# Performance work log

Measured on AMD Instinct MI355X. Metric: run time of the kernel, lower is better.

## Reference

```python
import jax, jax.numpy as jnp
import numpy as np

# levels for the auction iterations: j = 7..-1 gives level = -4^j, j = -2 gives level = 0
_LEVEL_JS = list(range(7, -3, -1))


def approx_match(xyz1, xyz2):
    # xyz1: [B,N,3], xyz2: [B,M,3] -> soft match matrix [B,N,M]
    B, N, _ = xyz1.shape
    M = xyz2.shape[1]
    multiL = 1.0 if N >= M else float(M // N)
    multiR = float(N // M) if N >= M else 1.0
    # pairwise squared distances [B,N,M]
    d2 = jnp.sum((xyz1[:, :, None, :] - xyz2[:, None, :, :]) ** 2, axis=-1)
    levels = jnp.array([0.0 if j == -2 else -(4.0 ** j) for j in _LEVEL_JS],
                       dtype=xyz1.dtype)

    def step(carry, level):
        match, remainL, remainR = carry
        w = jnp.exp(level * d2) * remainR[:, None, :]                      # [B,N,M]
        # row-normalize to each left point's remaining mass
        w = w * (remainL / (jnp.sum(w, axis=2) + 1e-9))[:, :, None]
        # clip columns to right points' remaining capacity
        ss = jnp.sum(w, axis=1) + 1e-9                                     # [B,M]
        w = w * jnp.minimum(remainR / ss, 1.0)[:, None, :]
        match = match + w
        remainL = jnp.maximum(remainL - jnp.sum(w, axis=2), 0.0)
        remainR = jnp.maximum(remainR - jnp.sum(w, axis=1), 0.0)
        return (match, remainL, remainR), None

    init = (jnp.zeros_like(d2),
            jnp.full((B, N), multiL, dtype=d2.dtype),
            jnp.full((B, M), multiR, dtype=d2.dtype))
    (match, _, _), _ = jax.lax.scan(step, init, levels)
    return match


def match_cost(xyz1, xyz2, match):
    # cost[b] = sum_{k,l} match[b,k,l] * ||xyz1[b,k] - xyz2[b,l]||
    d = jnp.sqrt(jnp.sum((xyz1[:, :, None, :] - xyz2[:, None, :, :]) ** 2, axis=-1))
    return jnp.sum(match * d, axis=(1, 2))


def setup_inputs() -> dict:
    key = jax.random.key(0)
    k1, k2 = jax.random.split(key)
    B, N, M = 8, 2048, 2048
    input1 = jax.random.normal(k1, (B, N, 3), dtype=jnp.float32)
    input2 = jax.random.normal(k2, (B, M, 3), dtype=jnp.float32)
    return {"input1": input1, "input2": input2}


def reference(input1, input2):
    match = approx_match(input1, input2)
    return match_cost(input1, input2, match)
```

## Files before the change

### kernel.cpp

```cpp
#include <hip/hip_runtime.h>
#include <hip/hip_fp16.h>


#define BATCH 8
#define NPTS 2048
#define MPTS 2048
#define BLOCK 256
#define ROWS 16
#define LOG2E 1.44269504088896340736f

__device__ __forceinline__ float fast_exp2(float x) {
  return __builtin_amdgcn_exp2f(x);
}
__device__ __forceinline__ float fast_sqrt(float a) {
  return __builtin_amdgcn_sqrtf(a);
}
__device__ __forceinline__ float packh2(float c, float r) {
  __half2 h = __halves2half2(__float2half_rn(c), __float2half_rn(r));
  return __builtin_bit_cast(float, h);
}

__device__ __forceinline__ void load8(const float4* q, int r0, float k,
                                      float* x, float* y, float* z) {
  int b4 = (r0 >> 2) * 3;
  float4 q0 = q[b4], q1 = q[b4 + 1], q2 = q[b4 + 2];
  float4 q3 = q[b4 + 3], q4 = q[b4 + 4], q5 = q[b4 + 5];
  x[0] = k * q0.x; y[0] = k * q0.y; z[0] = k * q0.z;
  x[1] = k * q0.w; y[1] = k * q1.x; z[1] = k * q1.y;
  x[2] = k * q1.z; y[2] = k * q1.w; z[2] = k * q2.x;
  x[3] = k * q2.y; y[3] = k * q2.z; z[3] = k * q2.w;
  x[4] = k * q3.x; y[4] = k * q3.y; z[4] = k * q3.z;
  x[5] = k * q3.w; y[5] = k * q4.x; z[5] = k * q4.y;
  x[6] = k * q4.z; y[6] = k * q4.w; z[6] = k * q5.x;
  x[7] = k * q5.y; y[7] = k * q5.z; z[7] = k * q5.w;
}

__global__ __launch_bounds__(BLOCK, 4) void emd_A0_kernel(
    const float* __restrict__ xyz1, const float* __restrict__ xyz2,
    float* __restrict__ rowscale, float* __restrict__ out,
    float* __restrict__ t9, float* __restrict__ t1acc,
    float* __restrict__ t1zero, float k0) {
  __shared__ float4 sP[MPTS];
  __shared__ float sRed[ROWS * 4];
  __shared__ float sRs[ROWS];

  const int tid = threadIdx.x;
  const int bid = blockIdx.x;
  const int b = bid >> 7;
  const int t0 = (bid & 127) * ROWS;
  const bool desig = (bid & 127) == 0;
  if (bid == 0 && tid < BATCH) { out[tid] = 0.0f; t9[tid] = 0.0f; }

  const float4* q2 = (const float4*)(xyz2 + (size_t)b * MPTS * 3);
  float4* z4 = (float4*)(t1zero + (size_t)b * MPTS);
  for (int g = tid; g < MPTS / 4; g += BLOCK) {
    float4 a = q2[3 * g], bb = q2[3 * g + 1], c = q2[3 * g + 2];
    sP[4 * g + 0] = make_float4(k0 * a.x, k0 * a.y, k0 * a.z, 0.0f);
    sP[4 * g + 1] = make_float4(k0 * a.w, k0 * bb.x, k0 * bb.y, 0.0f);
    sP[4 * g + 2] = make_float4(k0 * bb.z, k0 * bb.w, k0 * c.x, 0.0f);
    sP[4 * g + 3] = make_float4(k0 * c.y, k0 * c.z, k0 * c.w, 0.0f);
    if (desig) z4[g] = make_float4(0.f, 0.f, 0.f, 0.f);
  }
  __syncthreads();

  const int wave = tid >> 6, lane = tid & 63;
  const int phase = lane >> 1, rg = lane & 1;
  const int r0 = t0 + rg * 8;
  float x1[8], y1[8], z1[8], acc[8];
  load8((const float4*)(xyz1 + (size_t)b * NPTS * 3), r0, k0, x1, y1, z1);
#pragma unroll
  for (int j = 0; j < 8; ++j) acc[j] = 0.0f;
  const int mb = wave * 512 + phase;
#pragma unroll 2
  for (int it = 0; it < 16; ++it) {
    float4 v = sP[mb + it * 32];
#pragma unroll
    for (int j = 0; j < 8; ++j) {
      float dx = x1[j] - v.x, dy = y1[j] - v.y, dz = z1[j] - v.z;
      float s = __builtin_fmaf(dx, dx, __builtin_fmaf(dy, dy, dz * dz));
      acc[j] += fast_exp2(-s);
    }
  }
#pragma unroll
  for (int j = 0; j < 8; ++j) {
    acc[j] += __shfl_xor(acc[j], 2, 64);
    acc[j] += __shfl_xor(acc[j], 4, 64);
    acc[j] += __shfl_xor(acc[j], 8, 64);
    acc[j] += __shfl_xor(acc[j], 16, 64);
    acc[j] += __shfl_xor(acc[j], 32, 64);
  }
  if (lane < 2) {
#pragma unroll
    for (int j = 0; j < 8; ++j) sRed[(rg * 8 + j) * 4 + wave] = acc[j];
  }
  __syncthreads();
  if (tid < ROWS) {
    float s = sRed[tid * 4] + sRed[tid * 4 + 1] + sRed[tid * 4 + 2] +
              sRed[tid * 4 + 3];
    float rs = 1.0f / (s + 1e-9f);
    rowscale[(size_t)b * NPTS + t0 + tid] = rs;
    sRs[tid] = rs;
  }
  __syncthreads();

  float rsn[8];
#pragma unroll
  for (int j = 0; j < 8; ++j) rsn[j] = sRs[rg * 8 + j];
  float* accb = t1acc + (size_t)b * MPTS;
#pragma unroll 2
  for (int it = 0; it < 16; ++it) {
    int idx = mb + it * 32;
    float4 v = sP[idx];
    float part = 0.0f;
#pragma unroll
    for (int j = 0; j < 8; ++j) {
      float dx = x1[j] - v.x, dy = y1[j] - v.y, dz = z1[j] - v.z;
      float s = __builtin_fmaf(dx, dx, __builtin_fmaf(dy, dy, dz * dz));
      part = __builtin_fmaf(fast_exp2(-s), rsn[j], part);
    }
    part += __shfl_xor(part, 1, 64);
    if (rg == 0) atomicAdd(accb + idx, part);
  }
}

template <bool FIRST, bool LAST>
__global__ __launch_bounds__(BLOCK, 4) void emd_CA_kernel(
    const float* __restrict__ xyz1, const float* __restrict__ xyz2,
    float* __restrict__ rowscale, float* __restrict__ remainL,
    const float* __restrict__ rrIn, float* __restrict__ rrOut,
    const float* __restrict__ t1In, float* __restrict__ t1Acc,
    float* __restrict__ t1Zero, float* __restrict__ out,
    float* __restrict__ t9, float kS, float invK) {
  __shared__ float4 sP[MPTS];
  __shared__ float sRedS[ROWS * 4];
  __shared__ float sRedC[ROWS * 4];
  __shared__ float sRedR[ROWS * 4];
  __shared__ float sCost[ROWS];
  __shared__ float sRs[ROWS];

  const int tid = threadIdx.x;
  const int bid = blockIdx.x;
  const int b = bid >> 7;
  const int t0 = (bid & 127) * ROWS;
  const bool desig = (bid & 127) == 0;

  const float4* q2 = (const float4*)(xyz2 + (size_t)b * MPTS * 3);
  const float4* rr4 = (const float4*)(rrIn + (size_t)b * MPTS);
  const float4* t14 = (const float4*)(t1In + (size_t)b * MPTS);
  float4* ro4 = (float4*)(rrOut + (size_t)b * MPTS);
  float4* z4 = LAST ? nullptr : (float4*)(t1Zero + (size_t)b * MPTS);
  for (int g = tid; g < MPTS / 4; g += BLOCK) {
    float4 a = q2[3 * g], bb = q2[3 * g + 1], c = q2[3 * g + 2];
    float4 t1v = t14[g];
    float4 rrv = FIRST ? make_float4(1.f, 1.f, 1.f, 1.f) : rr4[g];
    float cc[4], rn[4];
    float rrc[4] = {rrv.x, rrv.y, rrv.z, rrv.w};
    float t1c[4] = {t1v.x, t1v.y, t1v.z, t1v.w};
#pragma unroll
    for (int i = 0; i < 4; ++i) {
      float colsum = rrc[i] * t1c[i];
      float cs = fminf(rrc[i] / (colsum + 1e-9f), 1.0f);
      cc[i] = rrc[i] * cs;
      rn[i] = fmaxf(rrc[i] - colsum * cs, 0.0f);
    }
    sP[4 * g + 0] = make_float4(kS * a.x, kS * a.y, kS * a.z, packh2(cc[0], rn[0]));
    sP[4 * g + 1] = make_float4(kS * a.w, kS * bb.x, kS * bb.y, packh2(cc[1], rn[1]));
    sP[4 * g + 2] = make_float4(kS * bb.z, kS * bb.w, kS * c.x, packh2(cc[2], rn[2]));
    sP[4 * g + 3] = make_float4(kS * c.y, kS * c.z, kS * c.w, packh2(cc[3], rn[3]));
    if (desig) {
      ro4[g] = make_float4(rn[0], rn[1], rn[2], rn[3]);
      if (!LAST) z4[g] = make_float4(0.f, 0.f, 0.f, 0.f);
    }
  }
  __syncthreads();

  const int wave = tid >> 6, lane = tid & 63;
  const int phase = lane >> 2, rg = lane & 3;
  const int r0 = t0 + rg * 4;
  float x1[4], y1[4], z1[4];
  {
    const float4* q1 = (const float4*)(xyz1 + (size_t)b * NPTS * 3);
    int b4 = (r0 >> 2) * 3;
    float4 a = q1[b4], bb = q1[b4 + 1], c = q1[b4 + 2];
    x1[0] = kS * a.x;  y1[0] = kS * a.y;  z1[0] = kS * a.z;
    x1[1] = kS * a.w;  y1[1] = kS * bb.x; z1[1] = kS * bb.y;
    x1[2] = kS * bb.z; y1[2] = kS * bb.w; z1[2] = kS * c.x;
    x1[3] = kS * c.y;  y1[3] = kS * c.z;  z1[3] = kS * c.w;
  }
  float accS[4] = {0.f, 0.f, 0.f, 0.f};
  float accC[4] = {0.f, 0.f, 0.f, 0.f};
  float accR[4] = {0.f, 0.f, 0.f, 0.f};
  const int mb = wave * 512 + phase;
#pragma unroll 4
  for (int it = 0; it < 32; ++it) {
    float4 v = sP[mb + it * 16];
    __half2 h = __builtin_bit_cast(__half2, v.w);
    float cc = __low2float(h);
    float rr = __high2float(h);
#pragma unroll
    for (int j = 0; j < 4; ++j) {
      float dx = x1[j] - v.x, dy = y1[j] - v.y, dz = z1[j] - v.z;
      float s = __builtin_fmaf(dx, dx, __builtin_fmaf(dy, dy, dz * dz));
      float sq = fast_sqrt(s);
      float e1, e2;
      if (LAST) {
        e2 = 1.0f;
        e1 = fast_exp2(-s);
      } else {
        e2 = fast_exp2(-s);
        float e2s = e2 * e2;
        e1 = e2s * e2s;
      }
      float t = e1 * cc;
      accS[j] += t;
      accC[j] = __builtin_fmaf(t, sq, accC[j]);
      if (LAST) accR[j] += rr;
      else      accR[j] = __builtin_fmaf(e2, rr, accR[j]);
    }
  }
#pragma unroll
  for (int j = 0; j < 4; ++j) {
    accS[j] += __shfl_xor(accS[j], 4, 64);
    accS[j] += __shfl_xor(accS[j], 8, 64);
    accS[j] += __shfl_xor(accS[j], 16, 64);
    accS[j] += __shfl_xor(accS[j], 32, 64);
    accC[j] += __shfl_xor(accC[j], 4, 64);
    accC[j] += __shfl_xor(accC[j], 8, 64);
    accC[j] += __shfl_xor(accC[j], 16, 64);
    accC[j] += __shfl_xor(accC[j], 32, 64);
    accR[j] += __shfl_xor(accR[j], 4, 64);
    accR[j] += __shfl_xor(accR[j], 8, 64);
    accR[j] += __shfl_xor(accR[j], 16, 64);
    accR[j] += __shfl_xor(accR[j], 32, 64);
  }
  if (lane < 4) {
#pragma unroll
    for (int j = 0; j < 4; ++j) {
      sRedS[(rg * 4 + j) * 4 + wave] = accS[j];
      sRedC[(rg * 4 + j) * 4 + wave] = accC[j];
      sRedR[(rg * 4 + j) * 4 + wave] = accR[j];
    }
  }
  __syncthreads();
  if (tid < ROWS) {
    float S2 = sRedS[tid * 4] + sRedS[tid * 4 + 1] + sRedS[tid * 4 + 2] +
               sRedS[tid * 4 + 3];
    float C = sRedC[tid * 4] + sRedC[tid * 4 + 1] + sRedC[tid * 4 + 2] +
              sRedC[tid * 4 + 3];
    float R = sRedR[tid * 4] + sRedR[tid * 4 + 1] + sRedR[tid * 4 + 2] +
              sRedR[tid * 4 + 3];
    size_t idx = (size_t)b * NPTS + t0 + tid;
    float rs = rowscale[idx];
    float rl = FIRST ? 1.0f : remainL[idx];
    float rlN = fmaxf(rl - rs * S2, 0.0f);
    remainL[idx] = rlN;
    float rsN = rlN / (R + 1e-9f);
    rowscale[idx] = rsN;
    sCost[tid] = rs * C * invK;
    sRs[tid] = rsN;
  }
  __syncthreads();
  if (tid == 0) {
    float t = 0.0f;
#pragma unroll
    for (int i = 0; i < ROWS; ++i) t += sCost[i];
    atomicAdd(out + b, t);
    if (LAST) {
      float r = 0.0f;
#pragma unroll
      for (int i = 0; i < ROWS; ++i) r += sRs[i];
      atomicAdd(t9 + b, r);
    }
  }
  if (!LAST) {
    float rsn[4];
#pragma unroll
    for (int j = 0; j < 4; ++j) rsn[j] = sRs[rg * 4 + j];
    float* accb = t1Acc + (size_t)b * MPTS;
#pragma unroll 4
    for (int it = 0; it < 32; ++it) {
      int idx = mb + it * 16;
      float4 v = sP[idx];
      float part = 0.0f;
#pragma unroll
      for (int j = 0; j < 4; ++j) {
        float dx = x1[j] - v.x, dy = y1[j] - v.y, dz = z1[j] - v.z;
        float s = __builtin_fmaf(dx, dx, __builtin_fmaf(dy, dy, dz * dz));
        part = __builtin_fmaf(fast_exp2(-s), rsn[j], part);
      }
      part += __shfl_xor(part, 1, 64);
      part += __shfl_xor(part, 2, 64);
      if (rg == 0) atomicAdd(accb + idx, part);
    }
  }
}

__global__ __launch_bounds__(BLOCK, 4) void emd_C9_kernel(
    const float* __restrict__ xyz1, const float* __restrict__ xyz2,
    const float* __restrict__ rowscale, const float* __restrict__ remainR,
    const float* __restrict__ t9, float* __restrict__ out) {
  __shared__ float4 sP[MPTS];
  __shared__ float sRed[ROWS * 4];
  __shared__ float sCost[ROWS];

  const int tid = threadIdx.x;
  const int bid = blockIdx.x;
  const int b = bid >> 7;
  const int t0 = (bid & 127) * ROWS;
  const int wave = tid >> 6, lane = tid & 63;
  const float t1 = t9[b];

  const float4* q2 = (const float4*)(xyz2 + (size_t)b * MPTS * 3);
  const float4* rr4 = (const float4*)(remainR + (size_t)b * MPTS);
  for (int g = tid; g < MPTS / 4; g += BLOCK) {
    float4 a = q2[3 * g], bb = q2[3 * g + 1], c = q2[3 * g + 2];
    float4 rr = rr4[g];
    float w0 = rr.x * fminf(rr.x / (rr.x * t1 + 1e-9f), 1.0f);
    float w1 = rr.y * fminf(rr.y / (rr.y * t1 + 1e-9f), 1.0f);
    float w2 = rr.z * fminf(rr.z / (rr.z * t1 + 1e-9f), 1.0f);
    float w3 = rr.w * fminf(rr.w / (rr.w * t1 + 1e-9f), 1.0f);
    sP[4 * g + 0] = make_float4(a.x, a.y, a.z, w0);
    sP[4 * g + 1] = make_float4(a.w, bb.x, bb.y, w1);
    sP[4 * g + 2] = make_float4(bb.z, bb.w, c.x, w2);
    sP[4 * g + 3] = make_float4(c.y, c.z, c.w, w3);
  }
  __syncthreads();

  const int phase = lane >> 1, rg = lane & 1;
  const int r0 = t0 + rg * 8;
  float x1[8], y1[8], z1[8], acc[8];
  load8((const float4*)(xyz1 + (size_t)b * NPTS * 3), r0, 1.0f, x1, y1, z1);
#pragma unroll
  for (int j = 0; j < 8; ++j) acc[j] = 0.0f;
  const int mb = wave * 512 + phase;
#pragma unroll 2
  for (int it = 0; it < 16; ++it) {
    float4 v = sP[mb + it * 32];
#pragma unroll
    for (int j = 0; j < 8; ++j) {
      float dx = x1[j] - v.x, dy = y1[j] - v.y, dz = z1[j] - v.z;
      float d2 = __builtin_fmaf(dx, dx, __builtin_fmaf(dy, dy, dz * dz));
      acc[j] = __builtin_fmaf(fast_sqrt(d2), v.w, acc[j]);
    }
  }
#pragma unroll
  for (int j = 0; j < 8; ++j) {
    acc[j] += __shfl_xor(acc[j], 2, 64);
    acc[j] += __shfl_xor(acc[j], 4, 64);
    acc[j] += __shfl_xor(acc[j], 8, 64);
    acc[j] += __shfl_xor(acc[j], 16, 64);
    acc[j] += __shfl_xor(acc[j], 32, 64);
  }
  if (lane < 2) {
#pragma unroll
    for (int j = 0; j < 8; ++j) sRed[(rg * 8 + j) * 4 + wave] = acc[j];
  }
  __syncthreads();
  if (tid < ROWS) {
    float C = sRed[tid * 4] + sRed[tid * 4 + 1] + sRed[tid * 4 + 2] +
              sRed[tid * 4 + 3];
    sCost[tid] = rowscale[(size_t)b * NPTS + t0 + tid] * C;
  }
  __syncthreads();
  if (tid == 0) {
    float t = 0.0f;
#pragma unroll
    for (int i = 0; i < ROWS; ++i) t += sCost[i];
    atomicAdd(out + b, t);
  }
}

extern "C" void kernel_launch(void* const* d_in, const int* in_sizes, int n_in,
                              void* d_out, int out_size, void* d_ws, size_t ws_size,
                              hipStream_t stream) {
  const float* xyz1 = (const float*)d_in[0];
  const float* xyz2 = (const float*)d_in[1];
  float* out = (float*)d_out;
  float* ws = (float*)d_ws;

  const int BN = BATCH * NPTS, BM = BATCH * MPTS;
  float* remainL  = ws;
  float* rowscale = ws + BN;
  float* rrA      = ws + 2 * BN;
  float* rrB      = ws + 2 * BN + BM;
  float* t1b      = ws + 2 * BN + 2 * BM;
  float* t9       = ws + 2 * BN + 5 * BM;

  const float levels[9] = {-16384.f, -4096.f, -1024.f, -256.f, -64.f,
                           -16.f,    -4.f,    -1.f,    -0.25f};
  dim3 grid(BATCH * (NPTS / ROWS));

  hipMemsetAsync(t1b, 0, (size_t)BM * sizeof(float), stream);

  emd_A0_kernel<<<grid, BLOCK, 0, stream>>>(
      xyz1, xyz2, rowscale, out, t9, t1b , t1b + BM ,
      sqrtf(-levels[0] * LOG2E));

  for (int l = 0; l < 9; ++l) {
    float kB = sqrtf(-levels[l] * LOG2E);
    float kA = 0.5f * kB;
    float* cur = t1b + (size_t)(l % 3) * BM;
    float* nxt = t1b + (size_t)((l + 1) % 3) * BM;
    float* zer = t1b + (size_t)((l + 2) % 3) * BM;
    float* rin = (l % 2 == 0) ? rrA : rrB;
    float* rou = (l % 2 == 0) ? rrB : rrA;
    if (l == 0) {
      emd_CA_kernel<true, false><<<grid, BLOCK, 0, stream>>>(
          xyz1, xyz2, rowscale, remainL, rin, rou, cur, nxt, zer, out, t9,
          kA, 1.0f / kA);
    } else if (l < 8) {
      emd_CA_kernel<false, false><<<grid, BLOCK, 0, stream>>>(
          xyz1, xyz2, rowscale, remainL, rin, rou, cur, nxt, zer, out, t9,
          kA, 1.0f / kA);
    } else {
      emd_CA_kernel<false, true><<<grid, BLOCK, 0, stream>>>(
          xyz1, xyz2, rowscale, remainL, rin, rou, cur, nxt, zer, out, t9,
          kB, 1.0f / kB);
    }
  }
  emd_C9_kernel<<<grid, BLOCK, 0, stream>>>(xyz1, xyz2, rowscale, rrB, t9, out);
}
```

Baseline: 357.6 us.

## Fuse all auction levels into one persistent kernel with per-batch grid barriers

Replaces the chain of eleven kernel launches (A0, nine CA levels, C9) with a single persistent kernel. Blocks of the same batch synchronise through atomic counter barriers, and row scale and remaining-left mass stay in shared memory across levels instead of going through global memory. Cross-block data is read and written with agent-scope relaxed atomics. This removes launch gaps and some global traffic. In exchange it needs all 1024 blocks to be co-resident, which the launch bounds of four blocks per CU should allow on a 256-CU device. The spin barrier has a guard that could silently break out early, and there are no acquire/release fences.

```diff
diff --git a/kernel.cpp b/kernel.cpp
--- a/kernel.cpp
+++ b/kernel.cpp
@@ -7,6 +7,8 @@
 #define MPTS 2048
 #define BLOCK 256
 #define ROWS 16
+#define BLOCKS_PER_BATCH 128
+#define NSYNC 11
 #define LOG2E 1.44269504088896340736f
 
 __device__ __forceinline__ float fast_exp2(float x) {
@@ -20,353 +22,373 @@
   return __builtin_bit_cast(float, h);
 }
 
-__device__ __forceinline__ void load8(const float4* q, int r0, float k,
+__device__ __forceinline__ float cohLoad(const float* p) {
+  return __hip_atomic_load((float*)p, __ATOMIC_RELAXED,
+                           __HIP_MEMORY_SCOPE_AGENT);
+}
+__device__ __forceinline__ void cohStore(float* p, float v) {
+  __hip_atomic_store(p, v, __ATOMIC_RELAXED, __HIP_MEMORY_SCOPE_AGENT);
+}
+__device__ __forceinline__ float4 cohLoad4(const float4* p) {
+  const float* f = (const float*)p;
+  return make_float4(cohLoad(f), cohLoad(f + 1), cohLoad(f + 2),
+                     cohLoad(f + 3));
+}
+__device__ __forceinline__ void cohStore4(float4* p, float4 v) {
+  float* f = (float*)p;
+  cohStore(f, v.x); cohStore(f + 1, v.y);
+  cohStore(f + 2, v.z); cohStore(f + 3, v.w);
+}
+
+__device__ __forceinline__ void batch_barrier(unsigned* c) {
+  __syncthreads();
+  if (threadIdx.x == 0) {
+    unsigned old = __hip_atomic_fetch_add(c, 1u, __ATOMIC_RELAXED,
+                                          __HIP_MEMORY_SCOPE_AGENT);
+    unsigned target = (old / BLOCKS_PER_BATCH + 1u) * BLOCKS_PER_BATCH;
+    int guard = 0;
+    while (__hip_atomic_load(c, __ATOMIC_RELAXED,
+                             __HIP_MEMORY_SCOPE_AGENT) < target) {
+      __builtin_amdgcn_s_sleep(2);
+      if (++guard > (1 << 22)) break;
+    }
+  }
+  asm volatile("" ::: "memory");
+  __syncthreads();
+}
+
+__device__ __forceinline__ void load8(const float4* q, int r0,
                                       float* x, float* y, float* z) {
   int b4 = (r0 >> 2) * 3;
   float4 q0 = q[b4], q1 = q[b4 + 1], q2 = q[b4 + 2];
   float4 q3 = q[b4 + 3], q4 = q[b4 + 4], q5 = q[b4 + 5];
-  x[0] = k * q0.x; y[0] = k * q0.y; z[0] = k * q0.z;
-  x[1] = k * q0.w; y[1] = k * q1.x; z[1] = k * q1.y;
-  x[2] = k * q1.z; y[2] = k * q1.w; z[2] = k * q2.x;
-  x[3] = k * q2.y; y[3] = k * q2.z; z[3] = k * q2.w;
-  x[4] = k * q3.x; y[4] = k * q3.y; z[4] = k * q3.z;
-  x[5] = k * q3.w; y[5] = k * q4.x; z[5] = k * q4.y;
-  x[6] = k * q4.z; y[6] = k * q4.w; z[6] = k * q5.x;
-  x[7] = k * q5.y; y[7] = k * q5.z; z[7] = k * q5.w;
-}
-
-__global__ __launch_bounds__(BLOCK, 4) void emd_A0_kernel(
+  x[0] = q0.x; y[0] = q0.y; z[0] = q0.z;
+  x[1] = q0.w; y[1] = q1.x; z[1] = q1.y;
+  x[2] = q1.z; y[2] = q1.w; z[2] = q2.x;
+  x[3] = q2.y; y[3] = q2.z; z[3] = q2.w;
+  x[4] = q3.x; y[4] = q3.y; z[4] = q3.z;
+  x[5] = q3.w; y[5] = q4.x; z[5] = q4.y;
+  x[6] = q4.z; y[6] = q4.w; z[6] = q5.x;
+  x[7] = q5.y; y[7] = q5.z; z[7] = q5.w;
+}
+
+__global__ __launch_bounds__(BLOCK, 4) void emd_fused_kernel(
     const float* __restrict__ xyz1, const float* __restrict__ xyz2,
-    float* __restrict__ rowscale, float* __restrict__ out,
-    float* __restrict__ t9, float* __restrict__ t1acc,
-    float* __restrict__ t1zero, float k0) {
+    float* __restrict__ out, float* __restrict__ t1b,
+    float* __restrict__ rrA, float* __restrict__ rrB,
+    float* __restrict__ t9, unsigned* __restrict__ ctr) {
   __shared__ float4 sP[MPTS];
-  __shared__ float sRed[ROWS * 4];
-  __shared__ float sRs[ROWS];
+  __shared__ float sRedS[ROWS * 4];
+  __shared__ float sRedC[ROWS * 4];
+  __shared__ float sRedR[ROWS * 4];
+  __shared__ float sCost[ROWS];
+  __shared__ float sRowScale[ROWS];
+  __shared__ float sRemainL[ROWS];
+  __shared__ float sRn[4];
 
   const int tid = threadIdx.x;
   const int bid = blockIdx.x;
   const int b = bid >> 7;
   const int t0 = (bid & 127) * ROWS;
   const bool desig = (bid & 127) == 0;
-  if (bid == 0 && tid < BATCH) { out[tid] = 0.0f; t9[tid] = 0.0f; }
-
-  const float4* q2 = (const float4*)(xyz2 + (size_t)b * MPTS * 3);
-  float4* z4 = (float4*)(t1zero + (size_t)b * MPTS);
-  for (int g = tid; g < MPTS / 4; g += BLOCK) {
-    float4 a = q2[3 * g], bb = q2[3 * g + 1], c = q2[3 * g + 2];
-    sP[4 * g + 0] = make_float4(k0 * a.x, k0 * a.y, k0 * a.z, 0.0f);
-    sP[4 * g + 1] = make_float4(k0 * a.w, k0 * bb.x, k0 * bb.y, 0.0f);
-    sP[4 * g + 2] = make_float4(k0 * bb.z, k0 * bb.w, k0 * c.x, 0.0f);
-    sP[4 * g + 3] = make_float4(k0 * c.y, k0 * c.z, k0 * c.w, 0.0f);
-    if (desig) z4[g] = make_float4(0.f, 0.f, 0.f, 0.f);
+  const int wave = tid >> 6, lane = tid & 63;
+  const size_t bM = (size_t)b * MPTS;
+  unsigned* cb = ctr + b;
+
+  float* cur = t1b + bM;
+  float* nxt = t1b + (size_t)(BATCH * MPTS) + bM;
+  float* zer = t1b + (size_t)(2 * BATCH * MPTS) + bM;
+  float* rin = rrA + bM;
+  float* rou = rrB + bM;
+
+  const float4* q1 = (const float4*)(xyz1 + (size_t)b * NPTS * 3);
+  const float4* q2 = (const float4*)(xyz2 + bM * 3);
+
+  {
+    float4* z0 = (float4*)cur;
+    float4* z1 = (float4*)nxt;
+    const float4 zz = make_float4(0.f, 0.f, 0.f, 0.f);
+    for (int g = tid; g < MPTS / 4; g += BLOCK) {
+      float4 a = q2[3 * g], bb = q2[3 * g + 1], c = q2[3 * g + 2];
+      sP[4 * g + 0] = make_float4(a.x, a.y, a.z, 0.f);
+      sP[4 * g + 1] = make_float4(a.w, bb.x, bb.y, 0.f);
+      sP[4 * g + 2] = make_float4(bb.z, bb.w, c.x, 0.f);
+      sP[4 * g + 3] = make_float4(c.y, c.z, c.w, 0.f);
+      if (desig) { cohStore4(z0 + g, zz); cohStore4(z1 + g, zz); }
+    }
+    if (desig && tid == 0) { cohStore(out + b, 0.f); cohStore(t9 + b, 0.f); }
   }
   __syncthreads();
 
-  const int wave = tid >> 6, lane = tid & 63;
-  const int phase = lane >> 1, rg = lane & 1;
-  const int r0 = t0 + rg * 8;
-  float x1[8], y1[8], z1[8], acc[8];
-  load8((const float4*)(xyz1 + (size_t)b * NPTS * 3), r0, k0, x1, y1, z1);
-#pragma unroll
-  for (int j = 0; j < 8; ++j) acc[j] = 0.0f;
-  const int mb = wave * 512 + phase;
+  const float nc0 = -16384.0f * LOG2E;
+  {
+    const int ph = lane >> 1, rg = lane & 1;
+    float x1a[8], y1a[8], z1a[8], acc[8];
+    load8(q1, t0 + rg * 8, x1a, y1a, z1a);
+#pragma unroll
+    for (int j = 0; j < 8; ++j) acc[j] = 0.f;
+    const int mb = wave * 512 + ph;
 #pragma unroll 2
-  for (int it = 0; it < 16; ++it) {
-    float4 v = sP[mb + it * 32];
+    for (int it = 0; it < 16; ++it) {
+      float4 v = sP[mb + it * 32];
+#pragma unroll
+      for (int j = 0; j < 8; ++j) {
+        float dx = x1a[j] - v.x, dy = y1a[j] - v.y, dz = z1a[j] - v.z;
+        float d2 = __builtin_fmaf(dx, dx, __builtin_fmaf(dy, dy, dz * dz));
+        acc[j] += fast_exp2(nc0 * d2);
+      }
+    }
 #pragma unroll
     for (int j = 0; j < 8; ++j) {
-      float dx = x1[j] - v.x, dy = y1[j] - v.y, dz = z1[j] - v.z;
-      float s = __builtin_fmaf(dx, dx, __builtin_fmaf(dy, dy, dz * dz));
-      acc[j] += fast_exp2(-s);
-    }
-  }
-#pragma unroll
-  for (int j = 0; j < 8; ++j) {
-    acc[j] += __shfl_xor(acc[j], 2, 64);
-    acc[j] += __shfl_xor(acc[j], 4, 64);
-    acc[j] += __shfl_xor(acc[j], 8, 64);
-    acc[j] += __shfl_xor(acc[j], 16, 64);
-    acc[j] += __shfl_xor(acc[j], 32, 64);
-  }
-  if (lane < 2) {
-#pragma unroll
-    for (int j = 0; j < 8; ++j) sRed[(rg * 8 + j) * 4 + wave] = acc[j];
-  }
-  __syncthreads();
-  if (tid < ROWS) {
-    float s = sRed[tid * 4] + sRed[tid * 4 + 1] + sRed[tid * 4 + 2] +
-              sRed[tid * 4 + 3];
-    float rs = 1.0f / (s + 1e-9f);
-    rowscale[(size_t)b * NPTS + t0 + tid] = rs;
-    sRs[tid] = rs;
-  }
-  __syncthreads();
-
-  float rsn[8];
-#pragma unroll
-  for (int j = 0; j < 8; ++j) rsn[j] = sRs[rg * 8 + j];
-  float* accb = t1acc + (size_t)b * MPTS;
+      acc[j] += __shfl_xor(acc[j], 2, 64);
+      acc[j] += __shfl_xor(acc[j], 4, 64);
+      acc[j] += __shfl_xor(acc[j], 8, 64);
+      acc[j] += __shfl_xor(acc[j], 16, 64);
+      acc[j] += __shfl_xor(acc[j], 32, 64);
+    }
+    if (lane < 2) {
+#pragma unroll
+      for (int j = 0; j < 8; ++j) sRedS[(rg * 8 + j) * 4 + wave] = acc[j];
+    }
+    __syncthreads();
+    if (tid < ROWS) {
+      float s = sRedS[tid * 4] + sRedS[tid * 4 + 1] + sRedS[tid * 4 + 2] +
+                sRedS[tid * 4 + 3];
+      sRowScale[tid] = 1.0f / (s + 1e-9f);
+    }
+    batch_barrier(cb + 0 * BATCH);
+    float rsn[8];
+#pragma unroll
+    for (int j = 0; j < 8; ++j) rsn[j] = sRowScale[rg * 8 + j];
 #pragma unroll 2
-  for (int it = 0; it < 16; ++it) {
-    int idx = mb + it * 32;
-    float4 v = sP[idx];
-    float part = 0.0f;
-#pragma unroll
-    for (int j = 0; j < 8; ++j) {
-      float dx = x1[j] - v.x, dy = y1[j] - v.y, dz = z1[j] - v.z;
-      float s = __builtin_fmaf(dx, dx, __builtin_fmaf(dy, dy, dz * dz));
-      part = __builtin_fmaf(fast_exp2(-s), rsn[j], part);
-    }
-    part += __shfl_xor(part, 1, 64);
-    if (rg == 0) atomicAdd(accb + idx, part);
-  }
-}
-
-template <bool FIRST, bool LAST>
-__global__ __launch_bounds__(BLOCK, 4) void emd_CA_kernel(
-    const float* __restrict__ xyz1, const float* __restrict__ xyz2,
-    float* __restrict__ rowscale, float* __restrict__ remainL,
-    const float* __restrict__ rrIn, float* __restrict__ rrOut,
-    const float* __restrict__ t1In, float* __restrict__ t1Acc,
-    float* __restrict__ t1Zero, float* __restrict__ out,
-    float* __restrict__ t9, float kS, float invK) {
-  __shared__ float4 sP[MPTS];
-  __shared__ float sRedS[ROWS * 4];
-  __shared__ float sRedC[ROWS * 4];
-  __shared__ float sRedR[ROWS * 4];
-  __shared__ float sCost[ROWS];
-  __shared__ float sRs[ROWS];
-
-  const int tid = threadIdx.x;
-  const int bid = blockIdx.x;
-  const int b = bid >> 7;
-  const int t0 = (bid & 127) * ROWS;
-  const bool desig = (bid & 127) == 0;
-
-  const float4* q2 = (const float4*)(xyz2 + (size_t)b * MPTS * 3);
-  const float4* rr4 = (const float4*)(rrIn + (size_t)b * MPTS);
-  const float4* t14 = (const float4*)(t1In + (size_t)b * MPTS);
-  float4* ro4 = (float4*)(rrOut + (size_t)b * MPTS);
-  float4* z4 = LAST ? nullptr : (float4*)(t1Zero + (size_t)b * MPTS);
-  for (int g = tid; g < MPTS / 4; g += BLOCK) {
-    float4 a = q2[3 * g], bb = q2[3 * g + 1], c = q2[3 * g + 2];
-    float4 t1v = t14[g];
-    float4 rrv = FIRST ? make_float4(1.f, 1.f, 1.f, 1.f) : rr4[g];
-    float cc[4], rn[4];
-    float rrc[4] = {rrv.x, rrv.y, rrv.z, rrv.w};
-    float t1c[4] = {t1v.x, t1v.y, t1v.z, t1v.w};
-#pragma unroll
-    for (int i = 0; i < 4; ++i) {
-      float colsum = rrc[i] * t1c[i];
-      float cs = fminf(rrc[i] / (colsum + 1e-9f), 1.0f);
-      cc[i] = rrc[i] * cs;
-      rn[i] = fmaxf(rrc[i] - colsum * cs, 0.0f);
-    }
-    sP[4 * g + 0] = make_float4(kS * a.x, kS * a.y, kS * a.z, packh2(cc[0], rn[0]));
-    sP[4 * g + 1] = make_float4(kS * a.w, kS * bb.x, kS * bb.y, packh2(cc[1], rn[1]));
-    sP[4 * g + 2] = make_float4(kS * bb.z, kS * bb.w, kS * c.x, packh2(cc[2], rn[2]));
-    sP[4 * g + 3] = make_float4(kS * c.y, kS * c.z, kS * c.w, packh2(cc[3], rn[3]));
-    if (desig) {
-      ro4[g] = make_float4(rn[0], rn[1], rn[2], rn[3]);
-      if (!LAST) z4[g] = make_float4(0.f, 0.f, 0.f, 0.f);
-    }
-  }
-  __syncthreads();
-
-  const int wave = tid >> 6, lane = tid & 63;
-  const int phase = lane >> 2, rg = lane & 3;
-  const int r0 = t0 + rg * 4;
+    for (int it = 0; it < 16; ++it) {
+      int idx = mb + it * 32;
+      float4 v = sP[idx];
+      float part = 0.f;
+#pragma unroll
+      for (int j = 0; j < 8; ++j) {
+        float dx = x1a[j] - v.x, dy = y1a[j] - v.y, dz = z1a[j] - v.z;
+        float d2 = __builtin_fmaf(dx, dx, __builtin_fmaf(dy, dy, dz * dz));
+        part = __builtin_fmaf(fast_exp2(nc0 * d2), rsn[j], part);
+      }
+      part += __shfl_xor(part, 1, 64);
+      if (rg == 0) atomicAdd(cur + idx, part);
+    }
+  }
+  batch_barrier(cb + 1 * BATCH);
+
   float x1[4], y1[4], z1[4];
   {
-    const float4* q1 = (const float4*)(xyz1 + (size_t)b * NPTS * 3);
-    int b4 = (r0 >> 2) * 3;
+    int b4 = ((t0 + (lane & 3) * 4) >> 2) * 3;
     float4 a = q1[b4], bb = q1[b4 + 1], c = q1[b4 + 2];
-    x1[0] = kS * a.x;  y1[0] = kS * a.y;  z1[0] = kS * a.z;
-    x1[1] = kS * a.w;  y1[1] = kS * bb.x; z1[1] = kS * bb.y;
-    x1[2] = kS * bb.z; y1[2] = kS * bb.w; z1[2] = kS * c.x;
-    x1[3] = kS * c.y;  y1[3] = kS * c.z;  z1[3] = kS * c.w;
-  }
-  float accS[4] = {0.f, 0.f, 0.f, 0.f};
-  float accC[4] = {0.f, 0.f, 0.f, 0.f};
-  float accR[4] = {0.f, 0.f, 0.f, 0.f};
-  const int mb = wave * 512 + phase;
-#pragma unroll 4
-  for (int it = 0; it < 32; ++it) {
-    float4 v = sP[mb + it * 16];
-    __half2 h = __builtin_bit_cast(__half2, v.w);
-    float cc = __low2float(h);
-    float rr = __high2float(h);
-#pragma unroll
-    for (int j = 0; j < 4; ++j) {
-      float dx = x1[j] - v.x, dy = y1[j] - v.y, dz = z1[j] - v.z;
-      float s = __builtin_fmaf(dx, dx, __builtin_fmaf(dy, dy, dz * dz));
-      float sq = fast_sqrt(s);
-      float e1, e2;
+    x1[0] = a.x;  y1[0] = a.y;  z1[0] = a.z;
+    x1[1] = a.w;  y1[1] = bb.x; z1[1] = bb.y;
+    x1[2] = bb.z; y1[2] = bb.w; z1[2] = c.x;
+    x1[3] = c.y;  y1[3] = c.z;  z1[3] = c.w;
+  }
+  const int phc = lane >> 2, rgc = lane & 3;
+  const int mbc = wave * 512 + phc;
+
+  float nc2 = -4096.0f * LOG2E;
+  for (int l = 0; l < 9; ++l) {
+    const bool LAST = (l == 8);
+    float rnsum = 0.f;
+    {
+      const float4* t14 = (const float4*)cur;
+      const float4* rr4 = (const float4*)rin;
+      float4* ro4 = (float4*)rou;
+      float4* z4 = (float4*)zer;
+      const float4 zz = make_float4(0.f, 0.f, 0.f, 0.f);
+      for (int g = tid; g < MPTS / 4; g += BLOCK) {
+        float4 t1v = cohLoad4(t14 + g);
+        float4 rrv = (l == 0) ? make_float4(1.f, 1.f, 1.f, 1.f)
+                              : cohLoad4(rr4 + g);
+        float rrc[4] = {rrv.x, rrv.y, rrv.z, rrv.w};
+        float t1c[4] = {t1v.x, t1v.y, t1v.z, t1v.w};
+        float cc[4], rn[4];
+#pragma unroll
+        for (int i = 0; i < 4; ++i) {
+          float colsum = rrc[i] * t1c[i];
+          float cs = fminf(rrc[i] / (colsum + 1e-9f), 1.0f);
+          cc[i] = rrc[i] * cs;
+          rn[i] = fmaxf(rrc[i] - colsum * cs, 0.f);
+        }
+        rnsum += rn[0] + rn[1] + rn[2] + rn[3];
+        sP[4 * g + 0].w = packh2(cc[0], rn[0]);
+        sP[4 * g + 1].w = packh2(cc[1], rn[1]);
+        sP[4 * g + 2].w = packh2(cc[2], rn[2]);
+        sP[4 * g + 3].w = packh2(cc[3], rn[3]);
+        if (desig) {
+          cohStore4(ro4 + g, make_float4(rn[0], rn[1], rn[2], rn[3]));
+          if (!LAST) cohStore4(z4 + g, zz);
+        }
+      }
       if (LAST) {
-        e2 = 1.0f;
-        e1 = fast_exp2(-s);
-      } else {
-        e2 = fast_exp2(-s);
-        float e2s = e2 * e2;
-        e1 = e2s * e2s;
-      }
-      float t = e1 * cc;
-      accS[j] += t;
-      accC[j] = __builtin_fmaf(t, sq, accC[j]);
-      if (LAST) accR[j] += rr;
-      else      accR[j] = __builtin_fmaf(e2, rr, accR[j]);
-    }
-  }
-#pragma unroll
-  for (int j = 0; j < 4; ++j) {
-    accS[j] += __shfl_xor(accS[j], 4, 64);
-    accS[j] += __shfl_xor(accS[j], 8, 64);
-    accS[j] += __shfl_xor(accS[j], 16, 64);
-    accS[j] += __shfl_xor(accS[j], 32, 64);
-    accC[j] += __shfl_xor(accC[j], 4, 64);
-    accC[j] += __shfl_xor(accC[j], 8, 64);
-    accC[j] += __shfl_xor(accC[j], 16, 64);
-    accC[j] += __shfl_xor(accC[j], 32, 64);
-    accR[j] += __shfl_xor(accR[j], 4, 64);
-    accR[j] += __shfl_xor(accR[j], 8, 64);
-    accR[j] += __shfl_xor(accR[j], 16, 64);
-    accR[j] += __shfl_xor(accR[j], 32, 64);
-  }
-  if (lane < 4) {
-#pragma unroll
-    for (int j = 0; j < 4; ++j) {
-      sRedS[(rg * 4 + j) * 4 + wave] = accS[j];
-      sRedC[(rg * 4 + j) * 4 + wave] = accC[j];
-      sRedR[(rg * 4 + j) * 4 + wave] = accR[j];
-    }
-  }
-  __syncthreads();
-  if (tid < ROWS) {
-    float S2 = sRedS[tid * 4] + sRedS[tid * 4 + 1] + sRedS[tid * 4 + 2] +
-               sRedS[tid * 4 + 3];
-    float C = sRedC[tid * 4] + sRedC[tid * 4 + 1] + sRedC[tid * 4 + 2] +
-              sRedC[tid * 4 + 3];
-    float R = sRedR[tid * 4] + sRedR[tid * 4 + 1] + sRedR[tid * 4 + 2] +
-              sRedR[tid * 4 + 3];
-    size_t idx = (size_t)b * NPTS + t0 + tid;
-    float rs = rowscale[idx];
-    float rl = FIRST ? 1.0f : remainL[idx];
-    float rlN = fmaxf(rl - rs * S2, 0.0f);
-    remainL[idx] = rlN;
-    float rsN = rlN / (R + 1e-9f);
-    rowscale[idx] = rsN;
-    sCost[tid] = rs * C * invK;
-    sRs[tid] = rsN;
-  }
-  __syncthreads();
-  if (tid == 0) {
-    float t = 0.0f;
-#pragma unroll
-    for (int i = 0; i < ROWS; ++i) t += sCost[i];
-    atomicAdd(out + b, t);
-    if (LAST) {
-      float r = 0.0f;
-#pragma unroll
-      for (int i = 0; i < ROWS; ++i) r += sRs[i];
-      atomicAdd(t9 + b, r);
-    }
-  }
-  if (!LAST) {
-    float rsn[4];
-#pragma unroll
-    for (int j = 0; j < 4; ++j) rsn[j] = sRs[rg * 4 + j];
-    float* accb = t1Acc + (size_t)b * MPTS;
+        rnsum += __shfl_xor(rnsum, 1, 64);
+        rnsum += __shfl_xor(rnsum, 2, 64);
+        rnsum += __shfl_xor(rnsum, 4, 64);
+        rnsum += __shfl_xor(rnsum, 8, 64);
+        rnsum += __shfl_xor(rnsum, 16, 64);
+        rnsum += __shfl_xor(rnsum, 32, 64);
+        if (lane == 0) sRn[wave] = rnsum;
+      }
+    }
+    __syncthreads();
+    float accS[4] = {0.f, 0.f, 0.f, 0.f};
+    float accC[4] = {0.f, 0.f, 0.f, 0.f};
+    float accR[4] = {0.f, 0.f, 0.f, 0.f};
 #pragma unroll 4
     for (int it = 0; it < 32; ++it) {
-      int idx = mb + it * 16;
-      float4 v = sP[idx];
-      float part = 0.0f;
+      float4 v = sP[mbc + it * 16];
+      __half2 h = __builtin_bit_cast(__half2, v.w);
+      float cc = __low2float(h);
+      float rr = __high2float(h);
 #pragma unroll
       for (int j = 0; j < 4; ++j) {
         float dx = x1[j] - v.x, dy = y1[j] - v.y, dz = z1[j] - v.z;
-        float s = __builtin_fmaf(dx, dx, __builtin_fmaf(dy, dy, dz * dz));
-        part = __builtin_fmaf(fast_exp2(-s), rsn[j], part);
-      }
-      part += __shfl_xor(part, 1, 64);
-      part += __shfl_xor(part, 2, 64);
-      if (rg == 0) atomicAdd(accb + idx, part);
-    }
-  }
-}
-
-__global__ __launch_bounds__(BLOCK, 4) void emd_C9_kernel(
-    const float* __restrict__ xyz1, const float* __restrict__ xyz2,
-    const float* __restrict__ rowscale, const float* __restrict__ remainR,
-    const float* __restrict__ t9, float* __restrict__ out) {
-  __shared__ float4 sP[MPTS];
-  __shared__ float sRed[ROWS * 4];
-  __shared__ float sCost[ROWS];
-
-  const int tid = threadIdx.x;
-  const int bid = blockIdx.x;
-  const int b = bid >> 7;
-  const int t0 = (bid & 127) * ROWS;
-  const int wave = tid >> 6, lane = tid & 63;
-  const float t1 = t9[b];
-
-  const float4* q2 = (const float4*)(xyz2 + (size_t)b * MPTS * 3);
-  const float4* rr4 = (const float4*)(remainR + (size_t)b * MPTS);
-  for (int g = tid; g < MPTS / 4; g += BLOCK) {
-    float4 a = q2[3 * g], bb = q2[3 * g + 1], c = q2[3 * g + 2];
-    float4 rr = rr4[g];
-    float w0 = rr.x * fminf(rr.x / (rr.x * t1 + 1e-9f), 1.0f);
-    float w1 = rr.y * fminf(rr.y / (rr.y * t1 + 1e-9f), 1.0f);
-    float w2 = rr.z * fminf(rr.z / (rr.z * t1 + 1e-9f), 1.0f);
-    float w3 = rr.w * fminf(rr.w / (rr.w * t1 + 1e-9f), 1.0f);
-    sP[4 * g + 0] = make_float4(a.x, a.y, a.z, w0);
-    sP[4 * g + 1] = make_float4(a.w, bb.x, bb.y, w1);
-    sP[4 * g + 2] = make_float4(bb.z, bb.w, c.x, w2);
-    sP[4 * g + 3] = make_float4(c.y, c.z, c.w, w3);
-  }
-  __syncthreads();
-
-  const int phase = lane >> 1, rg = lane & 1;
-  const int r0 = t0 + rg * 8;
-  float x1[8], y1[8], z1[8], acc[8];
-  load8((const float4*)(xyz1 + (size_t)b * NPTS * 3), r0, 1.0f, x1, y1, z1);
-#pragma unroll
-  for (int j = 0; j < 8; ++j) acc[j] = 0.0f;
-  const int mb = wave * 512 + phase;
+        float d2 = __builtin_fmaf(dx, dx, __builtin_fmaf(dy, dy, dz * dz));
+        float sq = fast_sqrt(d2);
+        float e2 = fast_exp2(nc2 * d2);
+        float e2s = e2 * e2;
+        float e1 = e2s * e2s;
+        float t = e1 * cc;
+        accS[j] += t;
+        accC[j] = __builtin_fmaf(t, sq, accC[j]);
+        accR[j] = __builtin_fmaf(e2, rr, accR[j]);
+      }
+    }
+#pragma unroll
+    for (int j = 0; j < 4; ++j) {
+      accS[j] += __shfl_xor(accS[j], 4, 64);
+      accS[j] += __shfl_xor(accS[j], 8, 64);
+      accS[j] += __shfl_xor(accS[j], 16, 64);
+      accS[j] += __shfl_xor(accS[j], 32, 64);
+      accC[j] += __shfl_xor(accC[j], 4, 64);
+      accC[j] += __shfl_xor(accC[j], 8, 64);
+      accC[j] += __shfl_xor(accC[j], 16, 64);
+      accC[j] += __shfl_xor(accC[j], 32, 64);
+      accR[j] += __shfl_xor(accR[j], 4, 64);
+      accR[j] += __shfl_xor(accR[j], 8, 64);
+      accR[j] += __shfl_xor(accR[j], 16, 64);
+      accR[j] += __shfl_xor(accR[j], 32, 64);
+    }
+    if (lane < 4) {
+#pragma unroll
+      for (int j = 0; j < 4; ++j) {
+        sRedS[(rgc * 4 + j) * 4 + wave] = accS[j];
+        sRedC[(rgc * 4 + j) * 4 + wave] = accC[j];
+        sRedR[(rgc * 4 + j) * 4 + wave] = accR[j];
+      }
+    }
+    __syncthreads();
+    if (tid < ROWS) {
+      float S2 = sRedS[tid * 4] + sRedS[tid * 4 + 1] + sRedS[tid * 4 + 2] +
+                 sRedS[tid * 4 + 3];
+      float C = sRedC[tid * 4] + sRedC[tid * 4 + 1] + sRedC[tid * 4 + 2] +
+                sRedC[tid * 4 + 3];
+      float R = sRedR[tid * 4] + sRedR[tid * 4 + 1] + sRedR[tid * 4 + 2] +
+                sRedR[tid * 4 + 3];
+      if (LAST) R = sRn[0] + sRn[1] + sRn[2] + sRn[3];
+      float rs = sRowScale[tid];
+      float rl = (l == 0) ? 1.0f : sRemainL[tid];
+      float rlN = fmaxf(rl - rs * S2, 0.f);
+      sRemainL[tid] = rlN;
+      sRowScale[tid] = rlN / (R + 1e-9f);
+      sCost[tid] = rs * C;
+    }
+    __syncthreads();
+    if (tid == 0) {
+      float t = 0.f;
+#pragma unroll
+      for (int i = 0; i < ROWS; ++i) t += sCost[i];
+      atomicAdd(out + b, t);
+      if (LAST) {
+        float r = 0.f;
+#pragma unroll
+        for (int i = 0; i < ROWS; ++i) r += sRowScale[i];
+        atomicAdd(t9 + b, r);
+      }
+    }
+    if (!LAST) {
+      float rsn[4];
+#pragma unroll
+      for (int j = 0; j < 4; ++j) rsn[j] = sRowScale[rgc * 4 + j];
+#pragma unroll 4
+      for (int it = 0; it < 32; ++it) {
+        int idx = mbc + it * 16;
+        float4 v = sP[idx];
+        float part = 0.f;
+#pragma unroll
+        for (int j = 0; j < 4; ++j) {
+          float dx = x1[j] - v.x, dy = y1[j] - v.y, dz = z1[j] - v.z;
+          float d2 = __builtin_fmaf(dx, dx, __builtin_fmaf(dy, dy, dz * dz));
+          part = __builtin_fmaf(fast_exp2(nc2 * d2), rsn[j], part);
+        }
+        part += __shfl_xor(part, 1, 64);
+        part += __shfl_xor(part, 2, 64);
+        if (rgc == 0) atomicAdd(nxt + idx, part);
+      }
+    }
+    batch_barrier(cb + (2 + l) * BATCH);
+    if (!LAST) {
+      float* tp = cur; cur = nxt; nxt = zer; zer = tp;
+      float* tr = rin; rin = rou; rou = tr;
+      nc2 *= 0.25f;
+    }
+  }
+
+  {
+    const float t1 = cohLoad(t9 + b);
+    const float4* rr4 = (const float4*)rou;
+    for (int g = tid; g < MPTS / 4; g += BLOCK) {
+      float4 rr = cohLoad4(rr4 + g);
+      sP[4 * g + 0].w = rr.x * fminf(rr.x / (__builtin_fmaf(rr.x, t1, 1e-9f)), 1.0f);
+      sP[4 * g + 1].w = rr.y * fminf(rr.y / (__builtin_fmaf(rr.y, t1, 1e-9f)), 1.0f);
+      sP[4 * g + 2].w = rr.z * fminf(rr.z / (__builtin_fmaf(rr.z, t1, 1e-9f)), 1.0f);
+      sP[4 * g + 3].w = rr.w * fminf(rr.w / (__builtin_fmaf(rr.w, t1, 1e-9f)), 1.0f);
+    }
+    __syncthreads();
+    const int ph = lane >> 1, rg = lane & 1;
+    float x1a[8], y1a[8], z1a[8], acc[8];
+    load8(q1, t0 + rg * 8, x1a, y1a, z1a);
+#pragma unroll
+    for (int j = 0; j < 8; ++j) acc[j] = 0.f;
+    const int mb = wave * 512 + ph;
 #pragma unroll 2
-  for (int it = 0; it < 16; ++it) {
-    float4 v = sP[mb + it * 32];
+    for (int it = 0; it < 16; ++it) {
+      float4 v = sP[mb + it * 32];
+#pragma unroll
+      for (int j = 0; j < 8; ++j) {
+        float dx = x1a[j] - v.x, dy = y1a[j] - v.y, dz = z1a[j] - v.z;
+        float d2 = __builtin_fmaf(dx, dx, __builtin_fmaf(dy, dy, dz * dz));
+        acc[j] = __builtin_fmaf(fast_sqrt(d2), v.w, acc[j]);
+      }
+    }
 #pragma unroll
     for (int j = 0; j < 8; ++j) {
-      float dx = x1[j] - v.x, dy = y1[j] - v.y, dz = z1[j] - v.z;
-      float d2 = __builtin_fmaf(dx, dx, __builtin_fmaf(dy, dy, dz * dz));
-      acc[j] = __builtin_fmaf(fast_sqrt(d2), v.w, acc[j]);
-    }
-  }
-#pragma unroll
-  for (int j = 0; j < 8; ++j) {
-    acc[j] += __shfl_xor(acc[j], 2, 64);
-    acc[j] += __shfl_xor(acc[j], 4, 64);
-    acc[j] += __shfl_xor(acc[j], 8, 64);
-    acc[j] += __shfl_xor(acc[j], 16, 64);
-    acc[j] += __shfl_xor(acc[j], 32, 64);
-  }
-  if (lane < 2) {
-#pragma unroll
-    for (int j = 0; j < 8; ++j) sRed[(rg * 8 + j) * 4 + wave] = acc[j];
-  }
-  __syncthreads();
-  if (tid < ROWS) {
-    float C = sRed[tid * 4] + sRed[tid * 4 + 1] + sRed[tid * 4 + 2] +
-              sRed[tid * 4 + 3];
-    sCost[tid] = rowscale[(size_t)b * NPTS + t0 + tid] * C;
-  }
-  __syncthreads();
-  if (tid == 0) {
-    float t = 0.0f;
-#pragma unroll
-    for (int i = 0; i < ROWS; ++i) t += sCost[i];
-    atomicAdd(out + b, t);
+      acc[j] += __shfl_xor(acc[j], 2, 64);
+      acc[j] += __shfl_xor(acc[j], 4, 64);
+      acc[j] += __shfl_xor(acc[j], 8, 64);
+      acc[j] += __shfl_xor(acc[j], 16, 64);
+      acc[j] += __shfl_xor(acc[j], 32, 64);
+    }
+    if (lane < 2) {
+#pragma unroll
+      for (int j = 0; j < 8; ++j) sRedS[(rg * 8 + j) * 4 + wave] = acc[j];
+    }
+    __syncthreads();
+    if (tid < ROWS) {
+      float C = sRedS[tid * 4] + sRedS[tid * 4 + 1] + sRedS[tid * 4 + 2] +
+                sRedS[tid * 4 + 3];
+      sCost[tid] = sRowScale[tid] * C;
+    }
+    __syncthreads();
+    if (tid == 0) {
+      float t = 0.f;
+#pragma unroll
+      for (int i = 0; i < ROWS; ++i) t += sCost[i];
+      atomicAdd(out + b, t);
+    }
   }
 }
 
@@ -378,45 +400,17 @@
   float* out = (float*)d_out;
   float* ws = (float*)d_ws;
 
-  const int BN = BATCH * NPTS, BM = BATCH * MPTS;
-  float* remainL  = ws;
-  float* rowscale = ws + BN;
-  float* rrA      = ws + 2 * BN;
-  float* rrB      = ws + 2 * BN + BM;
-  float* t1b      = ws + 2 * BN + 2 * BM;
-  float* t9       = ws + 2 * BN + 5 * BM;
-
-  const float levels[9] = {-16384.f, -4096.f, -1024.f, -256.f, -64.f,
-                           -16.f,    -4.f,    -1.f,    -0.25f};
-  dim3 grid(BATCH * (NPTS / ROWS));
-
-  hipMemsetAsync(t1b, 0, (size_t)BM * sizeof(float), stream);
-
-  emd_A0_kernel<<<grid, BLOCK, 0, stream>>>(
-      xyz1, xyz2, rowscale, out, t9, t1b , t1b + BM ,
-      sqrtf(-levels[0] * LOG2E));
-
-  for (int l = 0; l < 9; ++l) {
-    float kB = sqrtf(-levels[l] * LOG2E);
-    float kA = 0.5f * kB;
-    float* cur = t1b + (size_t)(l % 3) * BM;
-    float* nxt = t1b + (size_t)((l + 1) % 3) * BM;
-    float* zer = t1b + (size_t)((l + 2) % 3) * BM;
-    float* rin = (l % 2 == 0) ? rrA : rrB;
-    float* rou = (l % 2 == 0) ? rrB : rrA;
-    if (l == 0) {
-      emd_CA_kernel<true, false><<<grid, BLOCK, 0, stream>>>(
-          xyz1, xyz2, rowscale, remainL, rin, rou, cur, nxt, zer, out, t9,
-          kA, 1.0f / kA);
-    } else if (l < 8) {
-      emd_CA_kernel<false, false><<<grid, BLOCK, 0, stream>>>(
-          xyz1, xyz2, rowscale, remainL, rin, rou, cur, nxt, zer, out, t9,
-          kA, 1.0f / kA);
-    } else {
-      emd_CA_kernel<false, true><<<grid, BLOCK, 0, stream>>>(
-          xyz1, xyz2, rowscale, remainL, rin, rou, cur, nxt, zer, out, t9,
-          kB, 1.0f / kB);
-    }
-  }
-  emd_C9_kernel<<<grid, BLOCK, 0, stream>>>(xyz1, xyz2, rowscale, rrB, t9, out);
-}
+  const int BM = BATCH * MPTS;
+  float* rrA = ws;
+  float* rrB = ws + BM;
+  float* t1b = ws + 2 * BM;
+  float* t9  = ws + 5 * BM;
+  unsigned* ctr = (unsigned*)(ws + 5 * BM + 16);
+
+  hipMemsetAsync(ctr, 0, NSYNC * BATCH * sizeof(unsigned), stream);
+
+  void* args[] = {(void*)&xyz1, (void*)&xyz2, (void*)&out, (void*)&t1b,
+                  (void*)&rrA, (void*)&rrB, (void*)&t9, (void*)&ctr};
+  hipLaunchKernel((const void*)emd_fused_kernel,
+                  dim3(BATCH * (NPTS / ROWS)), dim3(BLOCK), args, 0, stream);
+}
```

New measurement: 728.9 us. 2.04x slower.
